# Kernel optimization log

Measured on AMD Instinct MI355X. Metric: run time of the kernel, lower is better.

The kernel has to match this reference:

```python
import jax, jax.numpy as jnp
import numpy as np

N = 1048576   # total nodes across the mini-batch
D = 128       # node feature dim
B = 2048      # number of graphs (segments)


def setup_inputs() -> dict:
    key = jax.random.key(0)
    x = jax.random.normal(key, (N, D), dtype=jnp.float32)
    # sorted segment ids, every segment 0..B-1 non-empty (~512 nodes each)
    batch = ((jnp.arange(N, dtype=jnp.int64) * B) // N).astype(jnp.int32)
    return {"x": x, "batch": batch, "num_segments": B}


def reference(x, batch, num_segments):
    # Faithful to: for bi in range(batch.max()+1): out.append(x[batch==bi].max(0)[0])
    # expressed as a single-pass segment max (indices are sorted).
    return jax.ops.segment_max(x, batch, num_segments=num_segments,
                               indices_are_sorted=True)
```

## Files before the change

### kernel.cpp

```cpp
#include <hip/hip_runtime.h>
#include <math.h>


__global__ __launch_bounds__(256) void seg_max_kernel(
    const float* __restrict__ x, const int* __restrict__ batch,
    float* __restrict__ out, int N, int B) {
    const int seg = blockIdx.x;

    int lo = 0, hi = N;
    while (lo < hi) {
        int mid = (lo + hi) >> 1;
        if (batch[mid] < seg) lo = mid + 1; else hi = mid;
    }
    const int start = lo;
    hi = N;
    while (lo < hi) {
        int mid = (lo + hi) >> 1;
        if (batch[mid] <= seg) lo = mid + 1; else hi = mid;
    }
    const int end = lo;

    const int tid  = threadIdx.x;
    const int col4 = tid & 31;
    const int rg   = tid >> 5;

    float4 m = make_float4(-INFINITY, -INFINITY, -INFINITY, -INFINITY);
    const float4* __restrict__ x4 = reinterpret_cast<const float4*>(x);

    for (int r = start + rg; r < end; r += 8) {
        float4 v = x4[(size_t)r * 32 + col4];
        m.x = fmaxf(m.x, v.x);
        m.y = fmaxf(m.y, v.y);
        m.z = fmaxf(m.z, v.z);
        m.w = fmaxf(m.w, v.w);
    }

    __shared__ float4 smem[256];
    smem[tid] = m;
    __syncthreads();
    #pragma unroll
    for (int step = 128; step >= 32; step >>= 1) {
        if (tid < step) {
            float4 o = smem[tid + step];
            float4 c = smem[tid];
            c.x = fmaxf(c.x, o.x);
            c.y = fmaxf(c.y, o.y);
            c.z = fmaxf(c.z, o.z);
            c.w = fmaxf(c.w, o.w);
            smem[tid] = c;
        }
        __syncthreads();
    }
    if (tid < 32) {
        reinterpret_cast<float4*>(out)[(size_t)seg * 32 + tid] = smem[tid];
    }
}

extern "C" void kernel_launch(void* const* d_in, const int* in_sizes, int n_in,
                              void* d_out, int out_size, void* d_ws, size_t ws_size,
                              hipStream_t stream) {
    const float* x     = (const float*)d_in[0];
    const int*   batch = (const int*)d_in[1];
    float*       out   = (float*)d_out;

    const int D = 128;
    const int N = in_sizes[0] / D;
    const int B = out_size / D;

    seg_max_kernel<<<B, 256, 0, stream>>>(x, batch, out, N, B);
}
```

Baseline: 108.4 us.

## Precompute segment bounds in separate kernel and unroll max loop for more loads in flight

Moves the per-block binary searches into a small preceding kernel that writes the B+1 segment offsets into workspace. The main kernel then reads two ints instead of doing about 40 dependent global loads per block. The main loop is unrolled 4x with independent accumulators so more row loads are in flight, and launch bounds request 8 waves per EU. The cost is an extra kernel launch and a dependency on workspace size.

```diff
diff --git a/kernel.cpp b/kernel.cpp
--- a/kernel.cpp
+++ b/kernel.cpp
@@ -2,38 +2,57 @@
 #include <math.h>
 
 
-__global__ __launch_bounds__(256) void seg_max_kernel(
-    const float* __restrict__ x, const int* __restrict__ batch,
-    float* __restrict__ out, int N, int B) {
-    const int seg = blockIdx.x;
-
+__global__ __launch_bounds__(256) void find_bounds_kernel(
+    const int* __restrict__ batch, int* __restrict__ bounds, int N, int B) {
+    int b = blockIdx.x * 256 + threadIdx.x;
+    if (b > B) return;
+    if (b == B) { bounds[B] = N; return; }
     int lo = 0, hi = N;
     while (lo < hi) {
         int mid = (lo + hi) >> 1;
-        if (batch[mid] < seg) lo = mid + 1; else hi = mid;
+        if (batch[mid] < b) lo = mid + 1; else hi = mid;
     }
-    const int start = lo;
-    hi = N;
-    while (lo < hi) {
-        int mid = (lo + hi) >> 1;
-        if (batch[mid] <= seg) lo = mid + 1; else hi = mid;
-    }
-    const int end = lo;
+    bounds[b] = lo;
+}
+
+__device__ __forceinline__ float4 max4(float4 a, float4 b) {
+    a.x = fmaxf(a.x, b.x);
+    a.y = fmaxf(a.y, b.y);
+    a.z = fmaxf(a.z, b.z);
+    a.w = fmaxf(a.w, b.w);
+    return a;
+}
+
+__global__ __launch_bounds__(256, 8) void seg_max_kernel(
+    const float* __restrict__ x, const int* __restrict__ bounds,
+    float* __restrict__ out) {
+    const int seg   = blockIdx.x;
+    const int start = bounds[seg];
+    const int end   = bounds[seg + 1];
 
     const int tid  = threadIdx.x;
     const int col4 = tid & 31;
     const int rg   = tid >> 5;
 
-    float4 m = make_float4(-INFINITY, -INFINITY, -INFINITY, -INFINITY);
     const float4* __restrict__ x4 = reinterpret_cast<const float4*>(x);
+    const float4 ninf = make_float4(-INFINITY, -INFINITY, -INFINITY, -INFINITY);
+    float4 m0 = ninf, m1 = ninf, m2 = ninf, m3 = ninf;
 
-    for (int r = start + rg; r < end; r += 8) {
-        float4 v = x4[(size_t)r * 32 + col4];
-        m.x = fmaxf(m.x, v.x);
-        m.y = fmaxf(m.y, v.y);
-        m.z = fmaxf(m.z, v.z);
-        m.w = fmaxf(m.w, v.w);
+    int r = start + rg;
+    for (; r + 24 < end; r += 32) {
+        float4 v0 = x4[(size_t)(r)      * 32 + col4];
+        float4 v1 = x4[(size_t)(r + 8)  * 32 + col4];
+        float4 v2 = x4[(size_t)(r + 16) * 32 + col4];
+        float4 v3 = x4[(size_t)(r + 24) * 32 + col4];
+        m0 = max4(m0, v0);
+        m1 = max4(m1, v1);
+        m2 = max4(m2, v2);
+        m3 = max4(m3, v3);
     }
+    for (; r < end; r += 8) {
+        m0 = max4(m0, x4[(size_t)r * 32 + col4]);
+    }
+    float4 m = max4(max4(m0, m1), max4(m2, m3));
 
     __shared__ float4 smem[256];
     smem[tid] = m;
@@ -41,13 +60,7 @@
     #pragma unroll
     for (int step = 128; step >= 32; step >>= 1) {
         if (tid < step) {
-            float4 o = smem[tid + step];
-            float4 c = smem[tid];
-            c.x = fmaxf(c.x, o.x);
-            c.y = fmaxf(c.y, o.y);
-            c.z = fmaxf(c.z, o.z);
-            c.w = fmaxf(c.w, o.w);
-            smem[tid] = c;
+            smem[tid] = max4(smem[tid], smem[tid + step]);
         }
         __syncthreads();
     }
@@ -62,10 +75,12 @@
     const float* x     = (const float*)d_in[0];
     const int*   batch = (const int*)d_in[1];
     float*       out   = (float*)d_out;
+    int*         bounds = (int*)d_ws;
 
     const int D = 128;
     const int N = in_sizes[0] / D;
     const int B = out_size / D;
 
-    seg_max_kernel<<<B, 256, 0, stream>>>(x, batch, out, N, B);
+    find_bounds_kernel<<<(B + 1 + 255) / 256, 256, 0, stream>>>(batch, bounds, N, B);
+    seg_max_kernel<<<B, 256, 0, stream>>>(x, bounds, out);
 }
```

Result: faster. 105.3 us (-2.9%).
